# Kernel tuning notes

Measured on AMD Instinct MI355X. Metric: run time of the kernel, lower is better.

## Reference

```python
import itertools, math
import jax, jax.numpy as jnp
import numpy as np

N_QUBITS = 8
N_LAYERS = 2
D = 2 ** N_QUBITS
B = 16384
PAIRS = list(itertools.combinations(range(N_QUBITS), 2))
N_PAIRS = len(PAIRS)


def _static():
    s = np.arange(D)
    # ising_masks[p, s] = +1 if bits qi,qj of s differ else -1
    masks = np.stack([
        np.where((((s >> (N_QUBITS - 1 - qi)) & 1) ^ ((s >> (N_QUBITS - 1 - qj)) & 1)).astype(bool), 1.0, -1.0).astype(np.float32)
        for qi, qj in PAIRS])
    # z_signs[k, s] = +1 if bit k of s is 0 else -1
    zsig = np.stack([
        np.where(((s >> (N_QUBITS - 1 - k)) & 1).astype(bool), -1.0, 1.0).astype(np.float32)
        for k in range(N_QUBITS)])
    # CNOT is a permutation: src[i] = i ^ target_mask if ctrl bit of i set, else i
    cidx = np.empty((N_LAYERS, N_QUBITS, D), np.int32)
    for l in range(N_LAYERS):
        rng = l % (N_QUBITS - 1) + 1 if N_QUBITS > 1 else 1
        for ctrl in range(N_QUBITS):
            tgt = (ctrl + rng) % N_QUBITS
            bit = ((s >> (N_QUBITS - 1 - ctrl)) & 1).astype(bool)
            cidx[l, ctrl] = np.where(bit, s ^ (1 << (N_QUBITS - 1 - tgt)), s)
    return jnp.asarray(masks), jnp.asarray(zsig), jnp.asarray(cidx)

ISING_MASKS, Z_SIGNS, CNOT_IDX = _static()


def _ry(a):
    # a: [...] -> [..., 2, 2] complex64
    c, sn = jnp.cos(a * 0.5), jnp.sin(a * 0.5)
    return jnp.stack([jnp.stack([c, -sn], -1), jnp.stack([sn, c], -1)], -2).astype(jnp.complex64)


def _rz(a):
    h = a.astype(jnp.complex64) * 0.5
    z = jnp.zeros_like(h)
    return jnp.stack([jnp.stack([jnp.exp(-1j * h), z], -1), jnp.stack([z, jnp.exp(1j * h)], -1)], -2)


def _rot(w):
    # w: [3] = (phi, theta, omega) -> Rot = RZ(omega) @ RY(theta) @ RZ(phi), shape [2,2]
    return _rz(w[2]) @ _ry(w[1]) @ _rz(w[0])


def _apply_1q(state, gate, k):
    # state: [B, D]; gate: [B,2,2] (batched) or [2,2] (shared)
    Bs, Ds = state.shape
    hi, lo = 1 << k, 1 << (N_QUBITS - k - 1)
    s = state.reshape(Bs, hi, 2, lo)
    if gate.ndim == 3:
        s = jnp.einsum('bij,bhjl->bhil', gate, s)
    else:
        s = jnp.einsum('ij,bhjl->bhil', gate, s)
    return s.reshape(Bs, Ds)


def _forward(theta, phi_enc, j_upper, vqc_weights):
    Bs = theta.shape[0]
    state = jnp.zeros((Bs, D), jnp.complex64).at[:, 0].set(1.0)
    # encoding layer
    for k in range(N_QUBITS):
        state = _apply_1q(state, _ry(theta[:, k]), k)
        state = _apply_1q(state, _rz(phi_enc[:, k]), k)
    # IsingZZ: product over pairs of exp(0.5j*pi*J_p*mask_p) == exp of sum
    exponent = (0.5 * math.pi) * (j_upper @ ISING_MASKS)  # [B, D], real
    state = state * jnp.exp(1j * exponent.astype(jnp.complex64))
    for l in range(N_LAYERS):
        for k in range(N_QUBITS):
            state = _apply_1q(state, _rot(vqc_weights[l, k]), k)
        for k in range(N_QUBITS):
            # CNOT ring as gather permutation (same math as state @ cnot.mT)
            state = jnp.take(state, CNOT_IDX[l, k], axis=1)
        if l < N_LAYERS - 1:
            for k in range(N_QUBITS):
                state = _apply_1q(state, _ry(theta[:, k] * 0.5), k)
                state = _apply_1q(state, _rz(phi_enc[:, k] * 0.5), k)
    probs = jnp.abs(state) ** 2  # [B, D] float32
    return (probs @ Z_SIGNS.T).astype(theta.dtype)  # [B, N_QUBITS]


def setup_inputs() -> dict:
    key = jax.random.key(0)
    k1, k2, k3, k4 = jax.random.split(key, 4)
    return {
        'theta': jax.random.normal(k1, (B, N_QUBITS), jnp.float32),
        'phi_enc': jax.random.normal(k2, (B, N_QUBITS), jnp.float32),
        'j_upper': jax.random.normal(k3, (B, N_PAIRS), jnp.float32),
        'vqc_weights': jax.random.normal(k4, (N_LAYERS, N_QUBITS, 3), jnp.float32),
    }


def reference(theta, phi_enc, j_upper, vqc_weights):
    return _forward(theta, phi_enc, j_upper, vqc_weights)
```

## Files before the change

### kernel.cpp

```cpp
#include <hip/hip_runtime.h>


using f2 = __attribute__((ext_vector_type(2))) float;

__device__ __forceinline__ f2 cmul2(f2 w, f2 z) {
    f2 r;
    r.x = w.x * z.x - w.y * z.y;
    r.y = w.x * z.y + w.y * z.x;
    return r;
}
__device__ __forceinline__ f2 cmadd(f2 acc, f2 w, f2 z) {
    acc.x += w.x * z.x - w.y * z.y;
    acc.y += w.x * z.y + w.y * z.x;
    return acc;
}

__device__ __forceinline__ f2 shflx(f2 v, int m) {
    f2 r; r.x = __shfl_xor(v.x, m, 64); r.y = __shfl_xor(v.y, m, 64); return r;
}

__device__ __forceinline__ float uxor(float f, unsigned u) {
    return __uint_as_float(__float_as_uint(f) ^ u);
}

__device__ __forceinline__ f2 enc_sel(float t, float p, bool hi) {
    float s_, c_, sp_, cp_;
    __sincosf(t * 0.5f, &s_, &c_);
    __sincosf(p * 0.5f, &sp_, &cp_);
    const float m = hi ? s_ : c_;
    f2 r; r.x = m * cp_; r.y = hi ? m * sp_ : -m * sp_;
    return r;
}

template<int VREG, int VLANE, int UREG>
__device__ __forceinline__ void gateU(f2 (&s)[16],
                                      float g00r, float giP, float brP, float g01i)
{
    if constexpr (VLANE == 0) {
        constexpr int pivot = VREG & (-VREG);
        #pragma unroll
        for (int j = 0; j < 16; ++j) {
            if ((j & pivot) != 0) continue;
            const int j2 = j ^ VREG;
            const f2 x = s[j], y = s[j2];
            {
                const bool n = (__builtin_popcount(j & UREG) & 1) != 0;
                const float gi = n ? -giP : giP, br = n ? -brP : brP;
                s[j].x = fmaf(-g01i, y.y, fmaf(br, y.x, fmaf(-gi, x.y, g00r * x.x)));
                s[j].y = fmaf( g01i, y.x, fmaf(br, y.y, fmaf( gi, x.x, g00r * x.y)));
            }
            {
                const bool n = (__builtin_popcount(j2 & UREG) & 1) != 0;
                const float gi = n ? -giP : giP, br = n ? -brP : brP;
                s[j2].x = fmaf(-g01i, x.y, fmaf(br, x.x, fmaf(-gi, y.y, g00r * y.x)));
                s[j2].y = fmaf( g01i, x.x, fmaf(br, x.y, fmaf( gi, y.x, g00r * y.y)));
            }
        }
    } else if constexpr (VREG == 0) {
        #pragma unroll
        for (int j = 0; j < 16; ++j) {
            const f2 w = shflx(s[j], VLANE);
            const f2 x = s[j];
            const bool n = (__builtin_popcount(j & UREG) & 1) != 0;
            const float gi = n ? -giP : giP, br = n ? -brP : brP;
            s[j].x = fmaf(-g01i, w.y, fmaf(br, w.x, fmaf(-gi, x.y, g00r * x.x)));
            s[j].y = fmaf( g01i, w.x, fmaf(br, w.y, fmaf( gi, x.x, g00r * x.y)));
        }
    } else {
        constexpr int pivot = VREG & (-VREG);
        #pragma unroll
        for (int j = 0; j < 16; ++j) {
            if ((j & pivot) != 0) continue;
            const int j2 = j ^ VREG;
            const f2 p1 = shflx(s[j2], VLANE);
            const f2 p2 = shflx(s[j],  VLANE);
            const f2 x = s[j], y = s[j2];
            {
                const bool n = (__builtin_popcount(j & UREG) & 1) != 0;
                const float gi = n ? -giP : giP, br = n ? -brP : brP;
                s[j].x = fmaf(-g01i, p1.y, fmaf(br, p1.x, fmaf(-gi, x.y, g00r * x.x)));
                s[j].y = fmaf( g01i, p1.x, fmaf(br, p1.y, fmaf( gi, x.x, g00r * x.y)));
            }
            {
                const bool n = (__builtin_popcount(j2 & UREG) & 1) != 0;
                const float gi = n ? -giP : giP, br = n ? -brP : brP;
                s[j2].x = fmaf(-g01i, p2.y, fmaf(br, p2.x, fmaf(-gi, y.y, g00r * y.x)));
                s[j2].y = fmaf( g01i, p2.x, fmaf(br, p2.y, fmaf( gi, y.x, g00r * y.y)));
            }
        }
    }
}

#define ROT0(K, VR, VL, UR, SL) do {                                    \
    const float4 g_ = *reinterpret_cast<const float4*>(gates + (K)*4);  \
    gateU<VR, VL, UR>(s, g_.x, uxor(g_.y, SL), uxor(g_.z, SL), g_.w);   \
} while (0)

#define FUSED(K, VR, VL, UR, SL) do {                                   \
    const float4 g_ = *reinterpret_cast<const float4*>(gates + (8+(K))*4); \
    const f2 R00 = {g_.x, g_.y}, R01 = {g_.z, g_.w};                    \
    float c_, s_, cp_, sp_;                                             \
    __sincosf(th[K] * 0.25f, &s_, &c_);                                 \
    __sincosf(ph[K] * 0.25f, &sp_, &cp_);                               \
    const f2 E00 = { c_*cp_, -c_*sp_}, E10 = { s_*cp_,  s_*sp_};        \
    const f2 E01 = {-s_*cp_,  s_*sp_}, E11 = { c_*cp_,  c_*sp_};        \
    const f2 F00 = cmadd(cmul2(R00, E00), R01, E10);                    \
    const f2 F01 = cmadd(cmul2(R00, E01), R01, E11);                    \
    gateU<VR, VL, UR>(s, F00.x, uxor(F00.y, SL), uxor(F01.x, SL), F01.y); \
} while (0)

__global__ __launch_bounds__(64) void prep_gates(const float* __restrict__ w,
                                                 float* __restrict__ g)
{
    const int t = threadIdx.x;
    if (t < 16) {
        const float wph = w[t*3+0], wth = w[t*3+1], wom = w[t*3+2];
        float c_, s_, ca_, sa_, cb_, sb_;
        __sincosf(wth * 0.5f, &s_, &c_);
        __sincosf(0.5f * (wph + wom), &sa_, &ca_);
        __sincosf(0.5f * (wph - wom), &sb_, &cb_);
        float* o = g + t * 4;
        o[0] =  c_*ca_;  o[1] = -c_*sa_;
        o[2] = -s_*cb_;  o[3] = -s_*sb_;
    }
}

__global__ __launch_bounds__(64, 4) void vqc_kernel(
    const float* __restrict__ theta,
    const float* __restrict__ phi,
    const float* __restrict__ jup,
    const float* __restrict__ gates,
    float* __restrict__ out,
    int Btot)
{
    const int wid    = blockIdx.x;
    const int lane   = threadIdx.x & 63;
    const int lane16 = lane & 15;
    const int bq     = wid * 4 + (lane >> 4);
    const int b      = bq < Btot ? bq : Btot - 1;

    float th[8], ph[8];
    {
        const float4* t4 = reinterpret_cast<const float4*>(theta + (size_t)b * 8);
        const float4* p4 = reinterpret_cast<const float4*>(phi   + (size_t)b * 8);
        const float4 a = t4[0], c = t4[1], d = p4[0], e = p4[1];
        th[0]=a.x; th[1]=a.y; th[2]=a.z; th[3]=a.w;
        th[4]=c.x; th[5]=c.y; th[6]=c.z; th[7]=c.w;
        ph[0]=d.x; ph[1]=d.y; ph[2]=d.z; ph[3]=d.w;
        ph[4]=e.x; ph[5]=e.y; ph[6]=e.z; ph[7]=e.w;
    }

    const unsigned s8 = (unsigned)(lane16 & 8) << 28;
    const unsigned s4 = (unsigned)(lane16 & 4) << 29;
    const unsigned s2 = (unsigned)(lane16 & 2) << 30;
    const unsigned s1 = (unsigned)(lane16 & 1) << 31;
    const unsigned sC = s8 ^ s4;
    const unsigned sE = sC ^ s2;
    const unsigned sF = sE ^ s1;

    f2 P = enc_sel(th[4], ph[4], (lane16 & 8) != 0);
    P = cmul2(P, enc_sel(th[5], ph[5], (lane16 & 4) != 0));
    P = cmul2(P, enc_sel(th[6], ph[6], (lane16 & 2) != 0));
    P = cmul2(P, enc_sel(th[7], ph[7], (lane16 & 1) != 0));

    f2 m01[4], m23[4];
    {
        float s0, c0, sp0, cp0, s1_, c1_, sp1, cp1;
        __sincosf(th[0]*0.5f, &s0, &c0); __sincosf(ph[0]*0.5f, &sp0, &cp0);
        __sincosf(th[1]*0.5f, &s1_, &c1_); __sincosf(ph[1]*0.5f, &sp1, &cp1);
        const f2 A0={c0*cp0,-c0*sp0}, A1={s0*cp0,s0*sp0};
        const f2 B0={c1_*cp1,-c1_*sp1}, B1={s1_*cp1,s1_*sp1};
        #pragma unroll
        for (int a = 0; a < 4; ++a)
            m01[a] = cmul2((a & 2) ? A1 : A0, (a & 1) ? B1 : B0);
        __sincosf(th[2]*0.5f, &s0, &c0); __sincosf(ph[2]*0.5f, &sp0, &cp0);
        __sincosf(th[3]*0.5f, &s1_, &c1_); __sincosf(ph[3]*0.5f, &sp1, &cp1);
        const f2 C0={c0*cp0,-c0*sp0}, C1={s0*cp0,s0*sp0};
        const f2 D0={c1_*cp1,-c1_*sp1}, D1={s1_*cp1,s1_*sp1};
        #pragma unroll
        for (int a = 0; a < 4; ++a)
            m23[a] = cmul2((a & 2) ? C1 : C0, (a & 1) ? D1 : D0);
    }

    float c01, c02, c03, c12, c13, c23, Q0, Q1, Q2, Q3, LL;
    {
        const float4* J4 = reinterpret_cast<const float4*>(jup + (size_t)b * 28);
        const float z4 = (lane16 & 8) ? -1.f : 1.f;
        const float z5 = (lane16 & 4) ? -1.f : 1.f;
        const float z6 = (lane16 & 2) ? -1.f : 1.f;
        const float z7 = (lane16 & 1) ? -1.f : 1.f;
        const float4 x0 = J4[0], x1 = J4[1], x2 = J4[2], x3 = J4[3];
        const float4 x4 = J4[4], x5 = J4[5], x6 = J4[6];
        c01 = x0.x; c02 = x0.y; c03 = x0.z;
        Q0  = x0.w*z4 + x1.x*z5 + x1.y*z6 + x1.z*z7;
        c12 = x1.w; c13 = x2.x;
        Q1  = x2.y*z4 + x2.z*z5 + x2.w*z6 + x3.x*z7;
        c23 = x3.y;
        Q2  = x3.z*z4 + x3.w*z5 + x4.x*z6 + x4.y*z7;
        Q3  = x4.z*z4 + x4.w*z5 + x5.x*z6 + x5.y*z7;
        LL  = x5.z*(z4*z5) + x5.w*(z4*z6) + x6.x*(z4*z7)
            + x6.y*(z5*z6) + x6.z*(z5*z7) + x6.w*(z6*z7);
    }

    f2 s[16];
    constexpr float HPI = 1.5707963267948966f;
    #pragma unroll
    for (int j = 0; j < 16; ++j) {
        f2 u = cmul2(cmul2(m01[j >> 2], m23[j & 3]), P);
        float S = LL;
        S += ((__builtin_popcount(j & 0xC) & 1) ? -c01 : c01);
        S += ((__builtin_popcount(j & 0xA) & 1) ? -c02 : c02);
        S += ((__builtin_popcount(j & 0x9) & 1) ? -c03 : c03);
        S += ((__builtin_popcount(j & 0x6) & 1) ? -c12 : c12);
        S += ((__builtin_popcount(j & 0x5) & 1) ? -c13 : c13);
        S += ((__builtin_popcount(j & 0x3) & 1) ? -c23 : c23);
        S += ((j & 8) ? -Q0 : Q0);
        S += ((j & 4) ? -Q1 : Q1);
        S += ((j & 2) ? -Q2 : Q2);
        S += ((j & 1) ? -Q3 : Q3);
        float se, ce;
        __sincosf(-HPI * S, &se, &ce);
        s[j] = cmul2(u, (f2){ce, se});
    }

    ROT0(0, 0x8, 0x0, 0x8, 0u);
    ROT0(1, 0x4, 0x0, 0x4, 0u);
    ROT0(2, 0x2, 0x0, 0x2, 0u);
    ROT0(3, 0x1, 0x0, 0x1, 0u);
    ROT0(4, 0x0, 0x8, 0x0, s8);
    ROT0(5, 0x0, 0x4, 0x0, s4);
    ROT0(6, 0x0, 0x2, 0x0, s2);
    ROT0(7, 0x0, 0x1, 0x0, s1);

    FUSED(0, 0xC, 0x0, 0x7, sF);
    FUSED(1, 0x6, 0x0, 0xC, 0u);
    FUSED(2, 0x3, 0x0, 0xE, 0u);
    FUSED(3, 0x1, 0x8, 0xF, 0u);
    FUSED(4, 0x0, 0xC, 0xF, s8);
    FUSED(5, 0x0, 0x6, 0xF, sC);
    FUSED(6, 0x0, 0x3, 0xF, sE);
    FUSED(7, 0xC, 0x1, 0xF, sF);

    float p[16];
    #pragma unroll
    for (int j = 0; j < 16; ++j) p[j] = fmaf(s[j].y, s[j].y, s[j].x * s[j].x);
    #pragma unroll
    for (int st = 1; st < 16; st <<= 1) {
        #pragma unroll
        for (int j = 0; j < 16; ++j) {
            if ((j & st) != 0) continue;
            const float a = p[j], bb = p[j | st];
            p[j] = a + bb;  p[j | st] = a - bb;
        }
    }
    float o[8];
    o[0] = (__popc(lane16 & 0x6) & 1) ? -p[0xE] : p[0xE];
    o[1] = (__popc(lane16 & 0x3) & 1) ? -p[0xF] : p[0xF];
    o[2] = (__popc(lane16 & 0xF) & 1) ? -p[0x9] : p[0x9];
    o[3] = p[0x3];
    o[4] = (__popc(lane16 & 0x7) & 1) ? -p[0x6] : p[0x6];
    o[5] = (__popc(lane16 & 0xC) & 1) ? -p[0xC] : p[0xC];
    o[6] = (__popc(lane16 & 0x9) & 1) ? -p[0x9] : p[0x9];
    o[7] = (__popc(lane16 & 0x3) & 1) ? -p[0x3] : p[0x3];

    #pragma unroll
    for (int m = 1; m <= 8; m <<= 1) {
        #pragma unroll
        for (int q = 0; q < 8; ++q) o[q] += __shfl_xor(o[q], m, 64);
    }

    if (lane16 == 0 && bq < Btot) {
        float4* op = reinterpret_cast<float4*>(out + (size_t)bq * 8);
        op[0] = make_float4(o[0], o[1], o[2], o[3]);
        op[1] = make_float4(o[4], o[5], o[6], o[7]);
    }
}

extern "C" void kernel_launch(void* const* d_in, const int* in_sizes, int n_in,
                              void* d_out, int out_size, void* d_ws, size_t ws_size,
                              hipStream_t stream) {
    const float* theta = (const float*)d_in[0];
    const float* phi   = (const float*)d_in[1];
    const float* jup   = (const float*)d_in[2];
    const float* w     = (const float*)d_in[3];
    float* out   = (float*)d_out;
    float* gates = (float*)d_ws;

    const int B = in_sizes[0] / 8;
    hipLaunchKernelGGL(prep_gates, dim3(1), dim3(64), 0, stream, w, gates);

    const int blocks = (B + 3) / 4;
    hipLaunchKernelGGL(vqc_kernel, dim3(blocks), dim3(64), 0, stream,
                       theta, phi, jup, gates, out, B);
}
```

Measured before the change: 81.90 us.

## Spread each statevector over 32 lanes, fold gate prep in, use ds_swizzle

Each sample's 256-amplitude state is now split across 32 lanes holding 8 amplitudes each, instead of 16 lanes holding 16. This lowers register pressure and raises thread-level parallelism. The separate gate-prep kernel is removed: each 256-thread block computes the rotation gates into shared memory behind a barrier, saving a launch. Cross-lane exchanges now use ds_swizzle instead of shfl_xor. The cost is more cross-lane traffic, since five qubits now live across lanes, plus redundant gate-prep sincos work in every block.

```diff
diff --git a/kernel.cpp b/kernel.cpp
--- a/kernel.cpp
+++ b/kernel.cpp
@@ -2,6 +2,16 @@
 
 
 using f2 = __attribute__((ext_vector_type(2))) float;
+
+template<int M>
+__device__ __forceinline__ float swzf(float v) {
+    return __int_as_float(__builtin_amdgcn_ds_swizzle(__float_as_int(v),
+                                                      (M << 10) | 0x1F));
+}
+template<int M>
+__device__ __forceinline__ f2 swz(f2 v) {
+    f2 r; r.x = swzf<M>(v.x); r.y = swzf<M>(v.y); return r;
+}
 
 __device__ __forceinline__ f2 cmul2(f2 w, f2 z) {
     f2 r;
@@ -14,11 +24,6 @@
     acc.y += w.x * z.y + w.y * z.x;
     return acc;
 }
-
-__device__ __forceinline__ f2 shflx(f2 v, int m) {
-    f2 r; r.x = __shfl_xor(v.x, m, 64); r.y = __shfl_xor(v.y, m, 64); return r;
-}
-
 __device__ __forceinline__ float uxor(float f, unsigned u) {
     return __uint_as_float(__float_as_uint(f) ^ u);
 }
@@ -33,13 +38,13 @@
 }
 
 template<int VREG, int VLANE, int UREG>
-__device__ __forceinline__ void gateU(f2 (&s)[16],
+__device__ __forceinline__ void gateU(f2 (&s)[8],
                                       float g00r, float giP, float brP, float g01i)
 {
     if constexpr (VLANE == 0) {
         constexpr int pivot = VREG & (-VREG);
         #pragma unroll
-        for (int j = 0; j < 16; ++j) {
+        for (int j = 0; j < 8; ++j) {
             if ((j & pivot) != 0) continue;
             const int j2 = j ^ VREG;
             const f2 x = s[j], y = s[j2];
@@ -58,8 +63,8 @@
         }
     } else if constexpr (VREG == 0) {
         #pragma unroll
-        for (int j = 0; j < 16; ++j) {
-            const f2 w = shflx(s[j], VLANE);
+        for (int j = 0; j < 8; ++j) {
+            const f2 w = swz<VLANE>(s[j]);
             const f2 x = s[j];
             const bool n = (__builtin_popcount(j & UREG) & 1) != 0;
             const float gi = n ? -giP : giP, br = n ? -brP : brP;
@@ -69,11 +74,11 @@
     } else {
         constexpr int pivot = VREG & (-VREG);
         #pragma unroll
-        for (int j = 0; j < 16; ++j) {
+        for (int j = 0; j < 8; ++j) {
             if ((j & pivot) != 0) continue;
             const int j2 = j ^ VREG;
-            const f2 p1 = shflx(s[j2], VLANE);
-            const f2 p2 = shflx(s[j],  VLANE);
+            const f2 p1 = swz<VLANE>(s[j2]);
+            const f2 p2 = swz<VLANE>(s[j]);
             const f2 x = s[j], y = s[j2];
             {
                 const bool n = (__builtin_popcount(j & UREG) & 1) != 0;
@@ -91,53 +96,48 @@
     }
 }
 
-#define ROT0(K, VR, VL, UR, SL) do {                                    \
-    const float4 g_ = *reinterpret_cast<const float4*>(gates + (K)*4);  \
-    gateU<VR, VL, UR>(s, g_.x, uxor(g_.y, SL), uxor(g_.z, SL), g_.w);   \
+#define ROT0(K, VR, VL, UR, SL) do {                                       \
+    const float4 g_ = *reinterpret_cast<const float4*>(&gbuf[(K)*4]);      \
+    gateU<VR, VL, UR>(s, g_.x, uxor(g_.y, SL), uxor(g_.z, SL), g_.w);      \
 } while (0)
 
-#define FUSED(K, VR, VL, UR, SL) do {                                   \
-    const float4 g_ = *reinterpret_cast<const float4*>(gates + (8+(K))*4); \
-    const f2 R00 = {g_.x, g_.y}, R01 = {g_.z, g_.w};                    \
-    float c_, s_, cp_, sp_;                                             \
-    __sincosf(th[K] * 0.25f, &s_, &c_);                                 \
-    __sincosf(ph[K] * 0.25f, &sp_, &cp_);                               \
-    const f2 E00 = { c_*cp_, -c_*sp_}, E10 = { s_*cp_,  s_*sp_};        \
-    const f2 E01 = {-s_*cp_,  s_*sp_}, E11 = { c_*cp_,  c_*sp_};        \
-    const f2 F00 = cmadd(cmul2(R00, E00), R01, E10);                    \
-    const f2 F01 = cmadd(cmul2(R00, E01), R01, E11);                    \
-    gateU<VR, VL, UR>(s, F00.x, uxor(F00.y, SL), uxor(F01.x, SL), F01.y); \
+#define FUSED(K, VR, VL, UR, SL) do {                                      \
+    const float4 g_ = *reinterpret_cast<const float4*>(&gbuf[(8+(K))*4]);  \
+    const f2 R00 = {g_.x, g_.y}, R01 = {g_.z, g_.w};                       \
+    float c_, s_, cp_, sp_;                                                \
+    __sincosf(th[K] * 0.25f, &s_, &c_);                                    \
+    __sincosf(ph[K] * 0.25f, &sp_, &cp_);                                  \
+    const f2 E00 = { c_*cp_, -c_*sp_}, E10 = { s_*cp_,  s_*sp_};           \
+    const f2 E01 = {-s_*cp_,  s_*sp_}, E11 = { c_*cp_,  c_*sp_};           \
+    const f2 F00 = cmadd(cmul2(R00, E00), R01, E10);                       \
+    const f2 F01 = cmadd(cmul2(R00, E01), R01, E11);                       \
+    gateU<VR, VL, UR>(s, F00.x, uxor(F00.y, SL), uxor(F01.x, SL), F01.y);  \
 } while (0)
 
-__global__ __launch_bounds__(64) void prep_gates(const float* __restrict__ w,
-                                                 float* __restrict__ g)
+__global__ __launch_bounds__(256, 4) void vqc_kernel(
+    const float* __restrict__ theta,
+    const float* __restrict__ phi,
+    const float* __restrict__ jup,
+    const float* __restrict__ w,
+    float* __restrict__ out,
+    int Btot)
 {
-    const int t = threadIdx.x;
+    const int t      = threadIdx.x;
+    const int lane32 = t & 31;
+    const int bq     = blockIdx.x * 8 + (t >> 5);
+    const int b      = bq < Btot ? bq : Btot - 1;
+
+    __shared__ float gbuf[64];
     if (t < 16) {
         const float wph = w[t*3+0], wth = w[t*3+1], wom = w[t*3+2];
         float c_, s_, ca_, sa_, cb_, sb_;
         __sincosf(wth * 0.5f, &s_, &c_);
         __sincosf(0.5f * (wph + wom), &sa_, &ca_);
         __sincosf(0.5f * (wph - wom), &sb_, &cb_);
-        float* o = g + t * 4;
-        o[0] =  c_*ca_;  o[1] = -c_*sa_;
-        o[2] = -s_*cb_;  o[3] = -s_*sb_;
-    }
-}
-
-__global__ __launch_bounds__(64, 4) void vqc_kernel(
-    const float* __restrict__ theta,
-    const float* __restrict__ phi,
-    const float* __restrict__ jup,
-    const float* __restrict__ gates,
-    float* __restrict__ out,
-    int Btot)
-{
-    const int wid    = blockIdx.x;
-    const int lane   = threadIdx.x & 63;
-    const int lane16 = lane & 15;
-    const int bq     = wid * 4 + (lane >> 4);
-    const int b      = bq < Btot ? bq : Btot - 1;
+        gbuf[t*4+0] =  c_*ca_;  gbuf[t*4+1] = -c_*sa_;
+        gbuf[t*4+2] = -s_*cb_;  gbuf[t*4+3] = -s_*sb_;
+    }
+    __syncthreads();
 
     float th[8], ph[8];
     {
@@ -150,20 +150,23 @@
         ph[4]=e.x; ph[5]=e.y; ph[6]=e.z; ph[7]=e.w;
     }
 
-    const unsigned s8 = (unsigned)(lane16 & 8) << 28;
-    const unsigned s4 = (unsigned)(lane16 & 4) << 29;
-    const unsigned s2 = (unsigned)(lane16 & 2) << 30;
-    const unsigned s1 = (unsigned)(lane16 & 1) << 31;
-    const unsigned sC = s8 ^ s4;
-    const unsigned sE = sC ^ s2;
-    const unsigned sF = sE ^ s1;
-
-    f2 P = enc_sel(th[4], ph[4], (lane16 & 8) != 0);
-    P = cmul2(P, enc_sel(th[5], ph[5], (lane16 & 4) != 0));
-    P = cmul2(P, enc_sel(th[6], ph[6], (lane16 & 2) != 0));
-    P = cmul2(P, enc_sel(th[7], ph[7], (lane16 & 1) != 0));
-
-    f2 m01[4], m23[4];
+    const unsigned s16 = (unsigned)(lane32 & 16) << 27;
+    const unsigned s8  = (unsigned)(lane32 &  8) << 28;
+    const unsigned s4  = (unsigned)(lane32 &  4) << 29;
+    const unsigned s2  = (unsigned)(lane32 &  2) << 30;
+    const unsigned s1  = (unsigned)(lane32 &  1) << 31;
+    const unsigned s18 = s16 ^ s8;
+    const unsigned s1C = s18 ^ s4;
+    const unsigned s1E = s1C ^ s2;
+    const unsigned s1F = s1E ^ s1;
+
+    f2 P = enc_sel(th[3], ph[3], (lane32 & 16) != 0);
+    P = cmul2(P, enc_sel(th[4], ph[4], (lane32 & 8) != 0));
+    P = cmul2(P, enc_sel(th[5], ph[5], (lane32 & 4) != 0));
+    P = cmul2(P, enc_sel(th[6], ph[6], (lane32 & 2) != 0));
+    P = cmul2(P, enc_sel(th[7], ph[7], (lane32 & 1) != 0));
+
+    f2 m01[4], e20, e21;
     {
         float s0, c0, sp0, cp0, s1_, c1_, sp1, cp1;
         __sincosf(th[0]*0.5f, &s0, &c0); __sincosf(ph[0]*0.5f, &sp0, &cp0);
@@ -174,105 +177,100 @@
         for (int a = 0; a < 4; ++a)
             m01[a] = cmul2((a & 2) ? A1 : A0, (a & 1) ? B1 : B0);
         __sincosf(th[2]*0.5f, &s0, &c0); __sincosf(ph[2]*0.5f, &sp0, &cp0);
-        __sincosf(th[3]*0.5f, &s1_, &c1_); __sincosf(ph[3]*0.5f, &sp1, &cp1);
-        const f2 C0={c0*cp0,-c0*sp0}, C1={s0*cp0,s0*sp0};
-        const f2 D0={c1_*cp1,-c1_*sp1}, D1={s1_*cp1,s1_*sp1};
-        #pragma unroll
-        for (int a = 0; a < 4; ++a)
-            m23[a] = cmul2((a & 2) ? C1 : C0, (a & 1) ? D1 : D0);
-    }
-
-    float c01, c02, c03, c12, c13, c23, Q0, Q1, Q2, Q3, LL;
+        e20 = (f2){c0*cp0, -c0*sp0};
+        e21 = (f2){s0*cp0,  s0*sp0};
+    }
+
+    float c01, c02, c12, Q0, Q1, Q2, LL;
     {
         const float4* J4 = reinterpret_cast<const float4*>(jup + (size_t)b * 28);
-        const float z4 = (lane16 & 8) ? -1.f : 1.f;
-        const float z5 = (lane16 & 4) ? -1.f : 1.f;
-        const float z6 = (lane16 & 2) ? -1.f : 1.f;
-        const float z7 = (lane16 & 1) ? -1.f : 1.f;
+        const float z3 = (lane32 & 16) ? -1.f : 1.f;
+        const float z4 = (lane32 &  8) ? -1.f : 1.f;
+        const float z5 = (lane32 &  4) ? -1.f : 1.f;
+        const float z6 = (lane32 &  2) ? -1.f : 1.f;
+        const float z7 = (lane32 &  1) ? -1.f : 1.f;
         const float4 x0 = J4[0], x1 = J4[1], x2 = J4[2], x3 = J4[3];
         const float4 x4 = J4[4], x5 = J4[5], x6 = J4[6];
-        c01 = x0.x; c02 = x0.y; c03 = x0.z;
-        Q0  = x0.w*z4 + x1.x*z5 + x1.y*z6 + x1.z*z7;
-        c12 = x1.w; c13 = x2.x;
-        Q1  = x2.y*z4 + x2.z*z5 + x2.w*z6 + x3.x*z7;
-        c23 = x3.y;
-        Q2  = x3.z*z4 + x3.w*z5 + x4.x*z6 + x4.y*z7;
-        Q3  = x4.z*z4 + x4.w*z5 + x5.x*z6 + x5.y*z7;
-        LL  = x5.z*(z4*z5) + x5.w*(z4*z6) + x6.x*(z4*z7)
-            + x6.y*(z5*z6) + x6.z*(z5*z7) + x6.w*(z6*z7);
-    }
-
-    f2 s[16];
+        c01 = x0.x; c02 = x0.y; c12 = x1.w;
+        Q0 = x0.z*z3 + x0.w*z4 + x1.x*z5 + x1.y*z6 + x1.z*z7;
+        Q1 = x2.x*z3 + x2.y*z4 + x2.z*z5 + x2.w*z6 + x3.x*z7;
+        Q2 = x3.y*z3 + x3.z*z4 + x3.w*z5 + x4.x*z6 + x4.y*z7;
+        LL = x4.z*(z3*z4) + x4.w*(z3*z5) + x5.x*(z3*z6) + x5.y*(z3*z7)
+           + x5.z*(z4*z5) + x5.w*(z4*z6) + x6.x*(z4*z7)
+           + x6.y*(z5*z6) + x6.z*(z5*z7) + x6.w*(z6*z7);
+    }
+
+    f2 s[8];
     constexpr float HPI = 1.5707963267948966f;
     #pragma unroll
-    for (int j = 0; j < 16; ++j) {
-        f2 u = cmul2(cmul2(m01[j >> 2], m23[j & 3]), P);
+    for (int j = 0; j < 8; ++j) {
+        f2 u = cmul2(cmul2(m01[j >> 1], (j & 1) ? e21 : e20), P);
         float S = LL;
-        S += ((__builtin_popcount(j & 0xC) & 1) ? -c01 : c01);
-        S += ((__builtin_popcount(j & 0xA) & 1) ? -c02 : c02);
-        S += ((__builtin_popcount(j & 0x9) & 1) ? -c03 : c03);
-        S += ((__builtin_popcount(j & 0x6) & 1) ? -c12 : c12);
-        S += ((__builtin_popcount(j & 0x5) & 1) ? -c13 : c13);
-        S += ((__builtin_popcount(j & 0x3) & 1) ? -c23 : c23);
-        S += ((j & 8) ? -Q0 : Q0);
-        S += ((j & 4) ? -Q1 : Q1);
-        S += ((j & 2) ? -Q2 : Q2);
-        S += ((j & 1) ? -Q3 : Q3);
+        S += ((__builtin_popcount(j & 6) & 1) ? -c01 : c01);
+        S += ((__builtin_popcount(j & 5) & 1) ? -c02 : c02);
+        S += ((__builtin_popcount(j & 3) & 1) ? -c12 : c12);
+        S += ((j & 4) ? -Q0 : Q0);
+        S += ((j & 2) ? -Q1 : Q1);
+        S += ((j & 1) ? -Q2 : Q2);
         float se, ce;
         __sincosf(-HPI * S, &se, &ce);
         s[j] = cmul2(u, (f2){ce, se});
     }
 
-    ROT0(0, 0x8, 0x0, 0x8, 0u);
-    ROT0(1, 0x4, 0x0, 0x4, 0u);
-    ROT0(2, 0x2, 0x0, 0x2, 0u);
-    ROT0(3, 0x1, 0x0, 0x1, 0u);
-    ROT0(4, 0x0, 0x8, 0x0, s8);
-    ROT0(5, 0x0, 0x4, 0x0, s4);
-    ROT0(6, 0x0, 0x2, 0x0, s2);
-    ROT0(7, 0x0, 0x1, 0x0, s1);
-
-    FUSED(0, 0xC, 0x0, 0x7, sF);
-    FUSED(1, 0x6, 0x0, 0xC, 0u);
-    FUSED(2, 0x3, 0x0, 0xE, 0u);
-    FUSED(3, 0x1, 0x8, 0xF, 0u);
-    FUSED(4, 0x0, 0xC, 0xF, s8);
-    FUSED(5, 0x0, 0x6, 0xF, sC);
-    FUSED(6, 0x0, 0x3, 0xF, sE);
-    FUSED(7, 0xC, 0x1, 0xF, sF);
-
-    float p[16];
+    ROT0(0, 0x4, 0x00, 0x4, 0u);
+    ROT0(1, 0x2, 0x00, 0x2, 0u);
+    ROT0(2, 0x1, 0x00, 0x1, 0u);
+    ROT0(3, 0x0, 0x10, 0x0, s16);
+    ROT0(4, 0x0, 0x08, 0x0, s8);
+    ROT0(5, 0x0, 0x04, 0x0, s4);
+    ROT0(6, 0x0, 0x02, 0x0, s2);
+    ROT0(7, 0x0, 0x01, 0x0, s1);
+
+    FUSED(0, 0x6, 0x00, 0x3, s1F);
+    FUSED(1, 0x3, 0x00, 0x6, 0u);
+    FUSED(2, 0x1, 0x10, 0x7, 0u);
+    FUSED(3, 0x0, 0x18, 0x7, s16);
+    FUSED(4, 0x0, 0x0C, 0x7, s18);
+    FUSED(5, 0x0, 0x06, 0x7, s1C);
+    FUSED(6, 0x0, 0x03, 0x7, s1E);
+    FUSED(7, 0x6, 0x01, 0x7, s1F);
+
+    float p[8];
     #pragma unroll
-    for (int j = 0; j < 16; ++j) p[j] = fmaf(s[j].y, s[j].y, s[j].x * s[j].x);
+    for (int j = 0; j < 8; ++j) p[j] = fmaf(s[j].y, s[j].y, s[j].x * s[j].x);
     #pragma unroll
-    for (int st = 1; st < 16; st <<= 1) {
-        #pragma unroll
-        for (int j = 0; j < 16; ++j) {
+    for (int st = 1; st < 8; st <<= 1) {
+        #pragma unroll
+        for (int j = 0; j < 8; ++j) {
             if ((j & st) != 0) continue;
             const float a = p[j], bb = p[j | st];
             p[j] = a + bb;  p[j | st] = a - bb;
         }
     }
-    float o[8];
-    o[0] = (__popc(lane16 & 0x6) & 1) ? -p[0xE] : p[0xE];
-    o[1] = (__popc(lane16 & 0x3) & 1) ? -p[0xF] : p[0xF];
-    o[2] = (__popc(lane16 & 0xF) & 1) ? -p[0x9] : p[0x9];
-    o[3] = p[0x3];
-    o[4] = (__popc(lane16 & 0x7) & 1) ? -p[0x6] : p[0x6];
-    o[5] = (__popc(lane16 & 0xC) & 1) ? -p[0xC] : p[0xC];
-    o[6] = (__popc(lane16 & 0x9) & 1) ? -p[0x9] : p[0x9];
-    o[7] = (__popc(lane16 & 0x3) & 1) ? -p[0x3] : p[0x3];
-
-    #pragma unroll
-    for (int m = 1; m <= 8; m <<= 1) {
-        #pragma unroll
-        for (int q = 0; q < 8; ++q) o[q] += __shfl_xor(o[q], m, 64);
-    }
-
-    if (lane16 == 0 && bq < Btot) {
+    const unsigned s06 = s4 ^ s2;
+    const unsigned s13 = s16 ^ s2 ^ s1;
+    const unsigned s07 = s06 ^ s1;
+    const unsigned s0C = s8 ^ s4;
+    const unsigned s19 = s18 ^ s1;
+    float o0 = uxor(p[7], s06);
+    float o1 = uxor(p[7], s13);
+    float o2 = uxor(p[4], s1F);
+    float o3 = uxor(p[1], s16);
+    float o4 = uxor(p[3], s07);
+    float o5 = uxor(p[6], s0C);
+    float o6 = uxor(p[4], s19);
+    float o7 = uxor(p[1], s13);
+
+    #define REDSTEP(M) do { o0 += swzf<M>(o0); o1 += swzf<M>(o1);      \
+        o2 += swzf<M>(o2); o3 += swzf<M>(o3); o4 += swzf<M>(o4);       \
+        o5 += swzf<M>(o5); o6 += swzf<M>(o6); o7 += swzf<M>(o7); } while (0)
+    REDSTEP(1); REDSTEP(2); REDSTEP(4); REDSTEP(8); REDSTEP(16);
+    #undef REDSTEP
+
+    if (lane32 == 0 && bq < Btot) {
         float4* op = reinterpret_cast<float4*>(out + (size_t)bq * 8);
-        op[0] = make_float4(o[0], o[1], o[2], o[3]);
-        op[1] = make_float4(o[4], o[5], o[6], o[7]);
+        op[0] = make_float4(o0, o1, o2, o3);
+        op[1] = make_float4(o4, o5, o6, o7);
     }
 }
 
@@ -283,13 +281,10 @@
     const float* phi   = (const float*)d_in[1];
     const float* jup   = (const float*)d_in[2];
     const float* w     = (const float*)d_in[3];
-    float* out   = (float*)d_out;
-    float* gates = (float*)d_ws;
+    float* out = (float*)d_out;
 
     const int B = in_sizes[0] / 8;
-    hipLaunchKernelGGL(prep_gates, dim3(1), dim3(64), 0, stream, w, gates);
-
-    const int blocks = (B + 3) / 4;
-    hipLaunchKernelGGL(vqc_kernel, dim3(blocks), dim3(64), 0, stream,
-                       theta, phi, jup, gates, out, B);
-}
+    const int blocks = (B + 7) / 8;
+    hipLaunchKernelGGL(vqc_kernel, dim3(blocks), dim3(256), 0, stream,
+                       theta, phi, jup, w, out, B);
+}
```

New measurement: 81.92 us. Within noise of the previous version (+0.0%).

## Replace xor shuffles with DPP/swizzle and cut register pressure for higher occupancy

Applied to the files above, without the earlier changes.

Swaps the generic __shfl_xor lane exchanges (which lower to ds_bpermute) for DPP quad permutes for xor 1/2/3 and ds_swizzle for larger xor masks, in both the gate application and the final reduction. It also scopes the theta/phi arrays to the state-initialisation block and reloads per-qubit angles from global memory inside the fused gates, so fewer registers stay live, and raises the launch bound to 5 waves. The intent is to cut cross-lane exchange latency and allow more waves per SIMD. The risks are extra global/cache loads for the angles and possible spills under the tighter register budget.

```diff
diff --git a/kernel.cpp b/kernel.cpp
--- a/kernel.cpp
+++ b/kernel.cpp
@@ -2,6 +2,26 @@
 
 
 using f2 = __attribute__((ext_vector_type(2))) float;
+
+template<int M>
+__device__ __forceinline__ float xlf(float v) {
+    if constexpr (M == 1)
+        return __int_as_float(__builtin_amdgcn_update_dpp(
+            0, __float_as_int(v), 0xB1, 0xF, 0xF, true));
+    else if constexpr (M == 2)
+        return __int_as_float(__builtin_amdgcn_update_dpp(
+            0, __float_as_int(v), 0x4E, 0xF, 0xF, true));
+    else if constexpr (M == 3)
+        return __int_as_float(__builtin_amdgcn_update_dpp(
+            0, __float_as_int(v), 0x1B, 0xF, 0xF, true));
+    else
+        return __int_as_float(__builtin_amdgcn_ds_swizzle(
+            __float_as_int(v), (M << 10) | 0x1F));
+}
+template<int M>
+__device__ __forceinline__ f2 xl(f2 v) {
+    f2 r; r.x = xlf<M>(v.x); r.y = xlf<M>(v.y); return r;
+}
 
 __device__ __forceinline__ f2 cmul2(f2 w, f2 z) {
     f2 r;
@@ -14,11 +34,6 @@
     acc.y += w.x * z.y + w.y * z.x;
     return acc;
 }
-
-__device__ __forceinline__ f2 shflx(f2 v, int m) {
-    f2 r; r.x = __shfl_xor(v.x, m, 64); r.y = __shfl_xor(v.y, m, 64); return r;
-}
-
 __device__ __forceinline__ float uxor(float f, unsigned u) {
     return __uint_as_float(__float_as_uint(f) ^ u);
 }
@@ -59,7 +74,7 @@
     } else if constexpr (VREG == 0) {
         #pragma unroll
         for (int j = 0; j < 16; ++j) {
-            const f2 w = shflx(s[j], VLANE);
+            const f2 w = xl<VLANE>(s[j]);
             const f2 x = s[j];
             const bool n = (__builtin_popcount(j & UREG) & 1) != 0;
             const float gi = n ? -giP : giP, br = n ? -brP : brP;
@@ -72,8 +87,8 @@
         for (int j = 0; j < 16; ++j) {
             if ((j & pivot) != 0) continue;
             const int j2 = j ^ VREG;
-            const f2 p1 = shflx(s[j2], VLANE);
-            const f2 p2 = shflx(s[j],  VLANE);
+            const f2 p1 = xl<VLANE>(s[j2]);
+            const f2 p2 = xl<VLANE>(s[j]);
             const f2 x = s[j], y = s[j2];
             {
                 const bool n = (__builtin_popcount(j & UREG) & 1) != 0;
@@ -96,17 +111,18 @@
     gateU<VR, VL, UR>(s, g_.x, uxor(g_.y, SL), uxor(g_.z, SL), g_.w);   \
 } while (0)
 
-#define FUSED(K, VR, VL, UR, SL) do {                                   \
+#define FUSED(K, VR, VL, UR, SL) do {                                      \
     const float4 g_ = *reinterpret_cast<const float4*>(gates + (8+(K))*4); \
-    const f2 R00 = {g_.x, g_.y}, R01 = {g_.z, g_.w};                    \
-    float c_, s_, cp_, sp_;                                             \
-    __sincosf(th[K] * 0.25f, &s_, &c_);                                 \
-    __sincosf(ph[K] * 0.25f, &sp_, &cp_);                               \
-    const f2 E00 = { c_*cp_, -c_*sp_}, E10 = { s_*cp_,  s_*sp_};        \
-    const f2 E01 = {-s_*cp_,  s_*sp_}, E11 = { c_*cp_,  c_*sp_};        \
-    const f2 F00 = cmadd(cmul2(R00, E00), R01, E10);                    \
-    const f2 F01 = cmadd(cmul2(R00, E01), R01, E11);                    \
-    gateU<VR, VL, UR>(s, F00.x, uxor(F00.y, SL), uxor(F01.x, SL), F01.y); \
+    const f2 R00 = {g_.x, g_.y}, R01 = {g_.z, g_.w};                       \
+    const float thk = theta[b8 + (K)], phk = phi[b8 + (K)];                \
+    float c_, s_, cp_, sp_;                                                \
+    __sincosf(thk * 0.25f, &s_, &c_);                                      \
+    __sincosf(phk * 0.25f, &sp_, &cp_);                                    \
+    const f2 E00 = { c_*cp_, -c_*sp_}, E10 = { s_*cp_,  s_*sp_};           \
+    const f2 E01 = {-s_*cp_,  s_*sp_}, E11 = { c_*cp_,  c_*sp_};           \
+    const f2 F00 = cmadd(cmul2(R00, E00), R01, E10);                       \
+    const f2 F01 = cmadd(cmul2(R00, E01), R01, E11);                       \
+    gateU<VR, VL, UR>(s, F00.x, uxor(F00.y, SL), uxor(F01.x, SL), F01.y);  \
 } while (0)
 
 __global__ __launch_bounds__(64) void prep_gates(const float* __restrict__ w,
@@ -125,7 +141,7 @@
     }
 }
 
-__global__ __launch_bounds__(64, 4) void vqc_kernel(
+__global__ __launch_bounds__(64, 5) void vqc_kernel(
     const float* __restrict__ theta,
     const float* __restrict__ phi,
     const float* __restrict__ jup,
@@ -138,17 +154,7 @@
     const int lane16 = lane & 15;
     const int bq     = wid * 4 + (lane >> 4);
     const int b      = bq < Btot ? bq : Btot - 1;
-
-    float th[8], ph[8];
-    {
-        const float4* t4 = reinterpret_cast<const float4*>(theta + (size_t)b * 8);
-        const float4* p4 = reinterpret_cast<const float4*>(phi   + (size_t)b * 8);
-        const float4 a = t4[0], c = t4[1], d = p4[0], e = p4[1];
-        th[0]=a.x; th[1]=a.y; th[2]=a.z; th[3]=a.w;
-        th[4]=c.x; th[5]=c.y; th[6]=c.z; th[7]=c.w;
-        ph[0]=d.x; ph[1]=d.y; ph[2]=d.z; ph[3]=d.w;
-        ph[4]=e.x; ph[5]=e.y; ph[6]=e.z; ph[7]=e.w;
-    }
+    const size_t b8  = (size_t)b * 8;
 
     const unsigned s8 = (unsigned)(lane16 & 8) << 28;
     const unsigned s4 = (unsigned)(lane16 & 4) << 29;
@@ -157,30 +163,6 @@
     const unsigned sC = s8 ^ s4;
     const unsigned sE = sC ^ s2;
     const unsigned sF = sE ^ s1;
-
-    f2 P = enc_sel(th[4], ph[4], (lane16 & 8) != 0);
-    P = cmul2(P, enc_sel(th[5], ph[5], (lane16 & 4) != 0));
-    P = cmul2(P, enc_sel(th[6], ph[6], (lane16 & 2) != 0));
-    P = cmul2(P, enc_sel(th[7], ph[7], (lane16 & 1) != 0));
-
-    f2 m01[4], m23[4];
-    {
-        float s0, c0, sp0, cp0, s1_, c1_, sp1, cp1;
-        __sincosf(th[0]*0.5f, &s0, &c0); __sincosf(ph[0]*0.5f, &sp0, &cp0);
-        __sincosf(th[1]*0.5f, &s1_, &c1_); __sincosf(ph[1]*0.5f, &sp1, &cp1);
-        const f2 A0={c0*cp0,-c0*sp0}, A1={s0*cp0,s0*sp0};
-        const f2 B0={c1_*cp1,-c1_*sp1}, B1={s1_*cp1,s1_*sp1};
-        #pragma unroll
-        for (int a = 0; a < 4; ++a)
-            m01[a] = cmul2((a & 2) ? A1 : A0, (a & 1) ? B1 : B0);
-        __sincosf(th[2]*0.5f, &s0, &c0); __sincosf(ph[2]*0.5f, &sp0, &cp0);
-        __sincosf(th[3]*0.5f, &s1_, &c1_); __sincosf(ph[3]*0.5f, &sp1, &cp1);
-        const f2 C0={c0*cp0,-c0*sp0}, C1={s0*cp0,s0*sp0};
-        const f2 D0={c1_*cp1,-c1_*sp1}, D1={s1_*cp1,s1_*sp1};
-        #pragma unroll
-        for (int a = 0; a < 4; ++a)
-            m23[a] = cmul2((a & 2) ? C1 : C0, (a & 1) ? D1 : D0);
-    }
 
     float c01, c02, c03, c12, c13, c23, Q0, Q1, Q2, Q3, LL;
     {
@@ -203,24 +185,61 @@
     }
 
     f2 s[16];
-    constexpr float HPI = 1.5707963267948966f;
-    #pragma unroll
-    for (int j = 0; j < 16; ++j) {
-        f2 u = cmul2(cmul2(m01[j >> 2], m23[j & 3]), P);
-        float S = LL;
-        S += ((__builtin_popcount(j & 0xC) & 1) ? -c01 : c01);
-        S += ((__builtin_popcount(j & 0xA) & 1) ? -c02 : c02);
-        S += ((__builtin_popcount(j & 0x9) & 1) ? -c03 : c03);
-        S += ((__builtin_popcount(j & 0x6) & 1) ? -c12 : c12);
-        S += ((__builtin_popcount(j & 0x5) & 1) ? -c13 : c13);
-        S += ((__builtin_popcount(j & 0x3) & 1) ? -c23 : c23);
-        S += ((j & 8) ? -Q0 : Q0);
-        S += ((j & 4) ? -Q1 : Q1);
-        S += ((j & 2) ? -Q2 : Q2);
-        S += ((j & 1) ? -Q3 : Q3);
-        float se, ce;
-        __sincosf(-HPI * S, &se, &ce);
-        s[j] = cmul2(u, (f2){ce, se});
+    {
+        float th[8], ph[8];
+        {
+            const float4* t4 = reinterpret_cast<const float4*>(theta + b8);
+            const float4* p4 = reinterpret_cast<const float4*>(phi   + b8);
+            const float4 a = t4[0], c = t4[1], d = p4[0], e = p4[1];
+            th[0]=a.x; th[1]=a.y; th[2]=a.z; th[3]=a.w;
+            th[4]=c.x; th[5]=c.y; th[6]=c.z; th[7]=c.w;
+            ph[0]=d.x; ph[1]=d.y; ph[2]=d.z; ph[3]=d.w;
+            ph[4]=e.x; ph[5]=e.y; ph[6]=e.z; ph[7]=e.w;
+        }
+
+        f2 P = enc_sel(th[4], ph[4], (lane16 & 8) != 0);
+        P = cmul2(P, enc_sel(th[5], ph[5], (lane16 & 4) != 0));
+        P = cmul2(P, enc_sel(th[6], ph[6], (lane16 & 2) != 0));
+        P = cmul2(P, enc_sel(th[7], ph[7], (lane16 & 1) != 0));
+
+        f2 m01[4], m23[4];
+        {
+            float s0, c0, sp0, cp0, s1_, c1_, sp1, cp1;
+            __sincosf(th[0]*0.5f, &s0, &c0); __sincosf(ph[0]*0.5f, &sp0, &cp0);
+            __sincosf(th[1]*0.5f, &s1_, &c1_); __sincosf(ph[1]*0.5f, &sp1, &cp1);
+            const f2 A0={c0*cp0,-c0*sp0}, A1={s0*cp0,s0*sp0};
+            const f2 B0={c1_*cp1,-c1_*sp1}, B1={s1_*cp1,s1_*sp1};
+            #pragma unroll
+            for (int a = 0; a < 4; ++a)
+                m01[a] = cmul2((a & 2) ? A1 : A0, (a & 1) ? B1 : B0);
+            __sincosf(th[2]*0.5f, &s0, &c0); __sincosf(ph[2]*0.5f, &sp0, &cp0);
+            __sincosf(th[3]*0.5f, &s1_, &c1_); __sincosf(ph[3]*0.5f, &sp1, &cp1);
+            const f2 C0={c0*cp0,-c0*sp0}, C1={s0*cp0,s0*sp0};
+            const f2 D0={c1_*cp1,-c1_*sp1}, D1={s1_*cp1,s1_*sp1};
+            #pragma unroll
+            for (int a = 0; a < 4; ++a)
+                m23[a] = cmul2((a & 2) ? C1 : C0, (a & 1) ? D1 : D0);
+        }
+
+        constexpr float HPI = 1.5707963267948966f;
+        #pragma unroll
+        for (int j = 0; j < 16; ++j) {
+            f2 u = cmul2(cmul2(m01[j >> 2], m23[j & 3]), P);
+            float S = LL;
+            S += ((__builtin_popcount(j & 0xC) & 1) ? -c01 : c01);
+            S += ((__builtin_popcount(j & 0xA) & 1) ? -c02 : c02);
+            S += ((__builtin_popcount(j & 0x9) & 1) ? -c03 : c03);
+            S += ((__builtin_popcount(j & 0x6) & 1) ? -c12 : c12);
+            S += ((__builtin_popcount(j & 0x5) & 1) ? -c13 : c13);
+            S += ((__builtin_popcount(j & 0x3) & 1) ? -c23 : c23);
+            S += ((j & 8) ? -Q0 : Q0);
+            S += ((j & 4) ? -Q1 : Q1);
+            S += ((j & 2) ? -Q2 : Q2);
+            S += ((j & 1) ? -Q3 : Q3);
+            float se, ce;
+            __sincosf(-HPI * S, &se, &ce);
+            s[j] = cmul2(u, (f2){ce, se});
+        }
     }
 
     ROT0(0, 0x8, 0x0, 0x8, 0u);
@@ -264,10 +283,13 @@
     o[7] = (__popc(lane16 & 0x3) & 1) ? -p[0x3] : p[0x3];
 
     #pragma unroll
-    for (int m = 1; m <= 8; m <<= 1) {
-        #pragma unroll
-        for (int q = 0; q < 8; ++q) o[q] += __shfl_xor(o[q], m, 64);
-    }
+    for (int q = 0; q < 8; ++q) o[q] += xlf<1>(o[q]);
+    #pragma unroll
+    for (int q = 0; q < 8; ++q) o[q] += xlf<2>(o[q]);
+    #pragma unroll
+    for (int q = 0; q < 8; ++q) o[q] += xlf<4>(o[q]);
+    #pragma unroll
+    for (int q = 0; q < 8; ++q) o[q] += xlf<8>(o[q]);
 
     if (lane16 == 0 && bq < Btot) {
         float4* op = reinterpret_cast<float4*>(out + (size_t)bq * 8);
```

After: 84.77 us. +3.5%, slower.
